# Optimization experiments

Hardware: AMD Instinct MI355X
Metric: run time of the kernel (lower is better)

The kernel has to match this reference:

```python
import jax, jax.numpy as jnp
from jax import lax
import numpy as np

B, T, F = 64, 512, 128
H, L = 256, 128  # hidden_nodes, latent_dim
KEEP = 0.4       # 1 - dropout (dropout = 0.6)


def _lstm_layer(x, W, U, b, mask, return_sequences):
    """Keras-style LSTM (gate order i,f,g,o) with input dropout mask shared over time."""
    xd = x * mask[:, None, :]                       # [B,T,in] * [B,1,in]
    xz = jnp.einsum('bti,ig->btg', xd, W) + b        # [B,T,4H] precomputed input projections
    Hn = U.shape[0]

    def step(carry, xz_t):
        h, c = carry
        z = xz_t + h @ U                             # [B,4H]
        i, f, g, o = jnp.split(z, 4, axis=-1)
        i = jax.nn.sigmoid(i)
        f = jax.nn.sigmoid(f)
        g = jnp.tanh(g)
        o = jax.nn.sigmoid(o)
        c = f * c + i * g
        h = o * jnp.tanh(c)
        return (h, c), h

    init = (jnp.zeros((x.shape[0], Hn), x.dtype), jnp.zeros((x.shape[0], Hn), x.dtype))
    (h_last, _), hs = lax.scan(step, init, jnp.swapaxes(xz, 0, 1))
    return jnp.swapaxes(hs, 0, 1) if return_sequences else h_last


def setup_inputs() -> dict:
    key = jax.random.key(0)
    ks = jax.random.split(key, 16)

    def w(k, shape):
        fan_in = shape[0]
        return (jax.random.normal(k, shape, jnp.float32) / np.sqrt(fan_in)).astype(jnp.float32)

    def dmask(k, shape):
        return (jax.random.bernoulli(k, KEEP, shape).astype(jnp.float32) / KEEP)

    return {
        'x':  jax.random.normal(ks[0], (B, T, F), jnp.float32),
        'W0': w(ks[1], (F, 4 * H)), 'U0': w(ks[2], (H, 4 * H)), 'b0': jnp.zeros((4 * H,), jnp.float32),
        'W1': w(ks[3], (H, 4 * H)), 'U1': w(ks[4], (H, 4 * H)), 'b1': jnp.zeros((4 * H,), jnp.float32),
        'W2': w(ks[5], (H, 4 * L)), 'U2': w(ks[6], (L, 4 * L)), 'b2': jnp.zeros((4 * L,), jnp.float32),
        'm0': dmask(ks[7], (B, F)),
        'm1': dmask(ks[8], (B, H)),
        'm2': dmask(ks[9], (B, H)),
    }


def reference(x, W0, U0, b0, W1, U1, b1, W2, U2, b2, m0, m1, m2):
    h = _lstm_layer(x, W0, U0, b0, m0, return_sequences=True)   # input_layer
    h = _lstm_layer(h, W1, U1, b1, m1, return_sequences=True)   # hidden layer 0
    out = _lstm_layer(h, W2, U2, b2, m2, return_sequences=False)  # output_layer -> [B, latent_dim]
    return out
```

## Files before the change

### kernel.cpp

```cpp
#include <hip/hip_runtime.h>
#include <hip/hip_fp16.h>
#include <math.h>

#define B_ 64
#define T_ 512

typedef _Float16 h2_t __attribute__((ext_vector_type(2)));

__device__ __forceinline__ float fdot2u(unsigned int a, unsigned int b, float c) {
#if __has_builtin(__builtin_amdgcn_fdot2)
    return __builtin_amdgcn_fdot2(__builtin_bit_cast(h2_t, a),
                                  __builtin_bit_cast(h2_t, b), c, false);
#else
    const __half2 ah = __builtin_bit_cast(__half2, a);
    const __half2 bh = __builtin_bit_cast(__half2, b);
    const float2 af = __half22float2(ah), bf = __half22float2(bh);
    return c + af.x * bf.x + af.y * bf.y;
#endif
}
__device__ __forceinline__ unsigned int pack_h2(float x, float y) {
    const __half2 h = __float22half2_rn(make_float2(x, y));
    return __builtin_bit_cast(unsigned int, h);
}
__device__ __forceinline__ float ubits(unsigned int a) { return __builtin_bit_cast(float, a); }
__device__ __forceinline__ unsigned short f2h_bits(float x) {
    return __builtin_bit_cast(unsigned short, (_Float16)x);
}
__device__ __forceinline__ float h2f_bits(unsigned int bits) {
    return (float)__builtin_bit_cast(_Float16, (unsigned short)(bits & 0xffffu));
}

__device__ __forceinline__ float fsig(float z) { return 1.f / (1.f + __expf(-z)); }
__device__ __forceinline__ float ftanh(float z) {
    const float e = __expf(2.f * z);
    return 1.f - 2.f / (e + 1.f);
}

__device__ __forceinline__ void bar_lds() {
    asm volatile("s_waitcnt lgkmcnt(0)" ::: "memory");
    __builtin_amdgcn_s_barrier();
    asm volatile("" ::: "memory");
}

__global__ __launch_bounds__(256) void gemm_mask_f16(
    const float* __restrict__ A, const float* __restrict__ W,
    const float* __restrict__ bias, const float* __restrict__ mask,
    float* __restrict__ C, int M, int N, int K)
{
    const int TM = 64, TN = 64, TK = 32, KP = 16;
    __shared__ __align__(16) unsigned int As2[KP][68];
    __shared__ __align__(16) unsigned int Bs2[KP][68];

    const int tid = threadIdx.x;
    const int bn = blockIdx.x;
    const int bm = blockIdx.y;
    const int row0 = bm * TM;
    const int b = row0 / T_;

    const int ty = tid >> 4;
    const int tx = tid & 15;
    const int m0 = ty * 4;
    const int n0 = tx * 4;

    float acc[4][4];
#pragma unroll
    for (int i = 0; i < 4; i++)
#pragma unroll
        for (int j = 0; j < 4; j++) acc[i][j] = 0.f;

    for (int kk = 0; kk < K; kk += TK) {
        {
            const int m = tid >> 2;
            const int kq = (tid & 3) * 8;
            const float4 mv0 = *(const float4*)(mask + (size_t)b * K + kk + kq);
            const float4 mv1 = *(const float4*)(mask + (size_t)b * K + kk + kq + 4);
            const float4 a0 = *(const float4*)(A + (size_t)(row0 + m) * K + kk + kq);
            const float4 a1 = *(const float4*)(A + (size_t)(row0 + m) * K + kk + kq + 4);
            As2[kq / 2 + 0][m] = pack_h2(a0.x * mv0.x, a0.y * mv0.y);
            As2[kq / 2 + 1][m] = pack_h2(a0.z * mv0.z, a0.w * mv0.w);
            As2[kq / 2 + 2][m] = pack_h2(a1.x * mv1.x, a1.y * mv1.y);
            As2[kq / 2 + 3][m] = pack_h2(a1.z * mv1.z, a1.w * mv1.w);
        }
        {
            const int kp = tid >> 4;
            const int nq = (tid & 15) * 4;
            const float4 w0 = *(const float4*)(W + (size_t)(kk + 2 * kp) * N + bn * TN + nq);
            const float4 w1 = *(const float4*)(W + (size_t)(kk + 2 * kp + 1) * N + bn * TN + nq);
            uint4 pv;
            pv.x = pack_h2(w0.x, w1.x);
            pv.y = pack_h2(w0.y, w1.y);
            pv.z = pack_h2(w0.z, w1.z);
            pv.w = pack_h2(w0.w, w1.w);
            *(uint4*)&Bs2[kp][nq] = pv;
        }
        __syncthreads();

#pragma unroll
        for (int kp = 0; kp < KP; kp++) {
            const uint4 a4 = *(const uint4*)&As2[kp][m0];
            const uint4 b4 = *(const uint4*)&Bs2[kp][n0];
            acc[0][0] = fdot2u(a4.x, b4.x, acc[0][0]); acc[0][1] = fdot2u(a4.x, b4.y, acc[0][1]);
            acc[0][2] = fdot2u(a4.x, b4.z, acc[0][2]); acc[0][3] = fdot2u(a4.x, b4.w, acc[0][3]);
            acc[1][0] = fdot2u(a4.y, b4.x, acc[1][0]); acc[1][1] = fdot2u(a4.y, b4.y, acc[1][1]);
            acc[1][2] = fdot2u(a4.y, b4.z, acc[1][2]); acc[1][3] = fdot2u(a4.y, b4.w, acc[1][3]);
            acc[2][0] = fdot2u(a4.z, b4.x, acc[2][0]); acc[2][1] = fdot2u(a4.z, b4.y, acc[2][1]);
            acc[2][2] = fdot2u(a4.z, b4.z, acc[2][2]); acc[2][3] = fdot2u(a4.z, b4.w, acc[2][3]);
            acc[3][0] = fdot2u(a4.w, b4.x, acc[3][0]); acc[3][1] = fdot2u(a4.w, b4.y, acc[3][1]);
            acc[3][2] = fdot2u(a4.w, b4.z, acc[3][2]); acc[3][3] = fdot2u(a4.w, b4.w, acc[3][3]);
        }
        __syncthreads();
    }

    const float4 bv = *(const float4*)(bias + bn * TN + n0);
#pragma unroll
    for (int i = 0; i < 4; i++) {
        float4 v;
        v.x = acc[i][0] + bv.x;
        v.y = acc[i][1] + bv.y;
        v.z = acc[i][2] + bv.z;
        v.w = acc[i][3] + bv.w;
        *(float4*)&C[(size_t)(row0 + m0 + i) * N + bn * TN + n0] = v;
    }
}

template <int HN, bool F16>
__global__ __launch_bounds__(1024, 4) void lstm_rec_v16(
    const float* __restrict__ xz,
    const float* __restrict__ U,
    float* __restrict__ hout,
    float* __restrict__ out_last,
    unsigned int* __restrict__ hbuf)
{
    constexpr int GATES = 4 * HN;
    constexpr int COLS = HN;
    constexpr int CP = COLS / 2;
    constexpr int NKG = 1024 / CP;
    constexpr int KH = HN / NKG;
    constexpr int HB = HN / 4;
    constexpr int KWORDS = F16 ? HN / 2 : HN;
    constexpr int WPT = F16 ? KH / 2 : KH;
    constexpr int COLSP = COLS + 2;
    constexpr int NR = 3 * HB / 2;

    __shared__ __align__(16) unsigned int hW[KWORDS];
    __shared__ __align__(16) float zpS[NKG * COLSP];

    const int tid = threadIdx.x;
    const int q = blockIdx.x >> 6;
    const int b = blockIdx.x & 63;

    const int cp = tid % CP;
    const int kq = tid / CP;
    const int c0 = 2 * cp;
    const int group = c0 / HB;
    const int gcol = group * HN + q * HB + (c0 % HB);
    const int wbase = kq * WPT;

    uint2 ur[WPT];
#pragma unroll
    for (int j = 0; j < WPT; ++j) {
        const int w = wbase + j;
        if constexpr (F16) {
            const float2 r0 = *(const float2*)(U + (size_t)(2 * w) * GATES + gcol);
            const float2 r1 = *(const float2*)(U + (size_t)(2 * w + 1) * GATES + gcol);
            ur[j].x = pack_h2(r0.x, r1.x);
            ur[j].y = pack_h2(r0.y, r1.y);
        } else {
            const float2 r0 = *(const float2*)(U + (size_t)w * GATES + gcol);
            ur[j].x = __builtin_bit_cast(unsigned int, r0.x);
            ur[j].y = __builtin_bit_cast(unsigned int, r0.y);
        }
    }
#pragma unroll
    for (int j = 0; j < WPT; ++j)
        asm volatile("" : "+v"(ur[j].x), "+v"(ur[j].y));

    if (tid < KWORDS) hW[tid] = 0u;
    float cst = 0.f;

    const float* xzcell = xz + (size_t)b * T_ * GATES + q * HB + tid;
    float z4[4] = {0.f, 0.f, 0.f, 0.f};
    if (tid < HB) {
#pragma unroll
        for (int g = 0; g < 4; ++g) z4[g] = xzcell[(size_t)g * HN];
    }
    __syncthreads();

#pragma unroll 1
    for (int t = 0; t < T_; ++t) {
        float acc0 = 0.f, acc1 = 0.f;
#pragma unroll
        for (int j = 0; j < WPT; j += 4) {
            const int w = wbase + j;
            const uint4 hw4 = *(const uint4*)&hW[w];
            if constexpr (F16) {
                acc0 = fdot2u(ur[j + 0].x, hw4.x, acc0); acc1 = fdot2u(ur[j + 0].y, hw4.x, acc1);
                acc0 = fdot2u(ur[j + 1].x, hw4.y, acc0); acc1 = fdot2u(ur[j + 1].y, hw4.y, acc1);
                acc0 = fdot2u(ur[j + 2].x, hw4.z, acc0); acc1 = fdot2u(ur[j + 2].y, hw4.z, acc1);
                acc0 = fdot2u(ur[j + 3].x, hw4.w, acc0); acc1 = fdot2u(ur[j + 3].y, hw4.w, acc1);
            } else {
                acc0 += ubits(ur[j + 0].x) * ubits(hw4.x); acc1 += ubits(ur[j + 0].y) * ubits(hw4.x);
                acc0 += ubits(ur[j + 1].x) * ubits(hw4.y); acc1 += ubits(ur[j + 1].y) * ubits(hw4.y);
                acc0 += ubits(ur[j + 2].x) * ubits(hw4.z); acc1 += ubits(ur[j + 2].y) * ubits(hw4.z);
                acc0 += ubits(ur[j + 3].x) * ubits(hw4.w); acc1 += ubits(ur[j + 3].y) * ubits(hw4.w);
            }
        }
        *(float2*)&zpS[kq * COLSP + c0] = make_float2(acc0, acc1);
        bar_lds();

        const unsigned int tag = (unsigned int)(t + 1);
        unsigned int* hslot = hbuf + (size_t)(t & 1) * B_ * HN + b * HN;

        if (tid < HB) {
            float zg[4];
#pragma unroll
            for (int g = 0; g < 4; ++g) {
                float zs = z4[g];
#pragma unroll
                for (int r = 0; r < NKG; ++r) zs += zpS[r * COLSP + g * HB + tid];
                zg[g] = zs;
            }
            if (t + 1 < T_) {
#pragma unroll
                for (int g = 0; g < 4; ++g)
                    z4[g] = xzcell[(size_t)(t + 1) * GATES + (size_t)g * HN];
            }
            const float ig = fsig(zg[0]);
            const float fg = fsig(zg[1]);
            const float gg = ftanh(zg[2]);
            const float og = fsig(zg[3]);
            cst = fg * cst + ig * gg;
            const float hnew = og * ftanh(cst);

            if (hout) hout[((size_t)b * T_ + t) * HN + q * HB + tid] = hnew;
            if (t == T_ - 1) {
                if (out_last) out_last[(size_t)b * HN + q * HB + tid] = hnew;
            } else {
                const unsigned short h16 = f2h_bits(hnew);
                __hip_atomic_store(&hslot[q * HB + tid],
                                   ((unsigned int)tag << 16) | (unsigned int)h16,
                                   __ATOMIC_RELAXED, __HIP_MEMORY_SCOPE_AGENT);
                if constexpr (F16) {
                    reinterpret_cast<unsigned short*>(hW)[q * HB + tid] = h16;
                } else {
                    hW[q * HB + tid] = __builtin_bit_cast(unsigned int, hnew);
                }
            }
        } else if (tid >= 64 && tid < 64 + NR && t < T_ - 1) {
            const int idx = tid - 64;
            const int qp0 = q * (HB / 2);
            const int p = idx + (idx >= qp0 ? (HB / 2) : 0);
            const unsigned long long* hq = (const unsigned long long*)hslot;
            unsigned long long v = __hip_atomic_load(&hq[p],
                __ATOMIC_RELAXED, __HIP_MEMORY_SCOPE_AGENT);
            while (((v >> 16) & 0xffffu) != tag || (v >> 48) != tag)
                v = __hip_atomic_load(&hq[p],
                    __ATOMIC_RELAXED, __HIP_MEMORY_SCOPE_AGENT);
            if constexpr (F16) {
                hW[p] = (unsigned int)(v & 0xffffu) |
                        ((unsigned int)((v >> 32) & 0xffffu) << 16);
            } else {
                hW[2 * p + 0] = __builtin_bit_cast(unsigned int, h2f_bits((unsigned int)v));
                hW[2 * p + 1] = __builtin_bit_cast(unsigned int, h2f_bits((unsigned int)(v >> 32)));
            }
        }
        bar_lds();
    }
}

__global__ __launch_bounds__(1024, 4) void lstm_full_v18(
    const float* __restrict__ xz,
    const float* __restrict__ U,
    float* __restrict__ out_last)
{
    constexpr int HN = 128;
    constexpr int GATES = 512;
    constexpr int COLS = 512;
    constexpr int CP = COLS / 2;
    constexpr int NKG = 1024 / CP;
    constexpr int KH = HN / NKG;
    constexpr int WPT = KH;
    constexpr int KWORDS = HN;
    constexpr int COLSP = COLS + 2;

    __shared__ __align__(16) unsigned int hW[KWORDS];
    __shared__ __align__(16) float zpS[NKG * COLSP];

    const int tid = threadIdx.x;
    const int b = blockIdx.x;

    const int cp = tid % CP;
    const int kq = tid / CP;
    const int c0 = 2 * cp;
    const int wbase = kq * WPT;

    uint2 ur[WPT];
#pragma unroll
    for (int j = 0; j < WPT; ++j) {
        const int w = wbase + j;
        const float2 r0 = *(const float2*)(U + (size_t)w * GATES + c0);
        ur[j].x = __builtin_bit_cast(unsigned int, r0.x);
        ur[j].y = __builtin_bit_cast(unsigned int, r0.y);
    }
#pragma unroll
    for (int j = 0; j < WPT; ++j)
        asm volatile("" : "+v"(ur[j].x), "+v"(ur[j].y));

    if (tid < KWORDS) hW[tid] = 0u;
    float cst = 0.f;

    const float* xzcell = xz + (size_t)b * T_ * GATES + tid;
    float z4[4] = {0.f, 0.f, 0.f, 0.f};
    if (tid < HN) {
#pragma unroll
        for (int g = 0; g < 4; ++g) z4[g] = xzcell[g * HN];
    }
    __syncthreads();

#pragma unroll 1
    for (int t = 0; t < T_; ++t) {
        float acc0 = 0.f, acc1 = 0.f;
#pragma unroll
        for (int j = 0; j < WPT; j += 4) {
            const int w = wbase + j;
            const uint4 hw4 = *(const uint4*)&hW[w];
            acc0 += ubits(ur[j + 0].x) * ubits(hw4.x); acc1 += ubits(ur[j + 0].y) * ubits(hw4.x);
            acc0 += ubits(ur[j + 1].x) * ubits(hw4.y); acc1 += ubits(ur[j + 1].y) * ubits(hw4.y);
            acc0 += ubits(ur[j + 2].x) * ubits(hw4.z); acc1 += ubits(ur[j + 2].y) * ubits(hw4.z);
            acc0 += ubits(ur[j + 3].x) * ubits(hw4.w); acc1 += ubits(ur[j + 3].y) * ubits(hw4.w);
        }
        *(float2*)&zpS[kq * COLSP + c0] = make_float2(acc0, acc1);
        bar_lds();

        if (tid < HN) {
            float zg[4];
#pragma unroll
            for (int g = 0; g < 4; ++g) {
                float zs = z4[g];
#pragma unroll
                for (int r = 0; r < NKG; ++r) zs += zpS[r * COLSP + g * HN + tid];
                zg[g] = zs;
            }
            if (t + 1 < T_) {
#pragma unroll
                for (int g = 0; g < 4; ++g)
                    z4[g] = xzcell[(size_t)(t + 1) * GATES + g * HN];
            }
            const float ig = fsig(zg[0]);
            const float fg = fsig(zg[1]);
            const float gg = ftanh(zg[2]);
            const float og = fsig(zg[3]);
            cst = fg * cst + ig * gg;
            const float hnew = og * ftanh(cst);

            if (t == T_ - 1) {
                out_last[(size_t)b * HN + tid] = hnew;
            } else {
                hW[tid] = __builtin_bit_cast(unsigned int, hnew);
            }
        }
        bar_lds();
    }
}

extern "C" void kernel_launch(void* const* d_in, const int* in_sizes, int n_in,
                              void* d_out, int out_size, void* d_ws, size_t ws_size,
                              hipStream_t stream)
{
    const float* x  = (const float*)d_in[0];
    const float* W0 = (const float*)d_in[1];
    const float* U0 = (const float*)d_in[2];
    const float* b0 = (const float*)d_in[3];
    const float* W1 = (const float*)d_in[4];
    const float* U1 = (const float*)d_in[5];
    const float* b1 = (const float*)d_in[6];
    const float* W2 = (const float*)d_in[7];
    const float* U2 = (const float*)d_in[8];
    const float* b2 = (const float*)d_in[9];
    const float* m0 = (const float*)d_in[10];
    const float* m1 = (const float*)d_in[11];
    const float* m2 = (const float*)d_in[12];
    float* out = (float*)d_out;

    char* ws = (char*)d_ws;
    float* xz = (float*)ws;
    float* h0 = (float*)(ws + 134217728);
    float* h1 = (float*)(ws + 134217728 + 33554432);
    unsigned int* hb0 = (unsigned int*)(ws + 134217728 + 2 * 33554432);
    unsigned int* hb1 = hb0 + 2 * B_ * 256;

    const int M = B_ * T_;

    gemm_mask_f16<<<dim3(1024 / 64, M / 64), 256, 0, stream>>>(x, W0, b0, m0, xz, M, 1024, 128);
    lstm_rec_v16<256, true><<<256, 1024, 0, stream>>>(xz, U0, h0, nullptr, hb0);

    gemm_mask_f16<<<dim3(1024 / 64, M / 64), 256, 0, stream>>>(h0, W1, b1, m1, xz, M, 1024, 256);
    lstm_rec_v16<256, true><<<256, 1024, 0, stream>>>(xz, U1, h1, nullptr, hb1);

    gemm_mask_f16<<<dim3(512 / 64, M / 64), 256, 0, stream>>>(h1, W2, b2, m2, xz, M, 512, 256);
    lstm_full_v18<<<64, 1024, 0, stream>>>(xz, U2, out);
}
```

Before: 2.114 ms.

## Replace fdot2 input-projection GEMM with MFMA f16 matrix-core GEMM

Rewrites the masked input-projection GEMM to use MFMA 16x16x32 f16 instructions, with 128x128 block tiles split into four 64x64 wave tiles and a K-major LDS layout for both operands. The goal is to move the three large projection GEMMs off scalar packed-dot arithmetic and onto the matrix cores. The trade-offs are scattered 4-byte output stores in place of float4 stores, strided scalar loads of W, and fewer blocks per GEMM. The sequential recurrent kernels, which likely dominate total time, are unchanged.

```diff
diff --git a/kernel.cpp b/kernel.cpp
--- a/kernel.cpp
+++ b/kernel.cpp
@@ -6,6 +6,8 @@
 #define T_ 512
 
 typedef _Float16 h2_t __attribute__((ext_vector_type(2)));
+typedef _Float16 f16x8 __attribute__((ext_vector_type(8)));
+typedef float f32x4 __attribute__((ext_vector_type(4)));
 
 __device__ __forceinline__ float fdot2u(unsigned int a, unsigned int b, float c) {
 #if __has_builtin(__builtin_amdgcn_fdot2)
@@ -42,84 +44,100 @@
     asm volatile("" ::: "memory");
 }
 
-__global__ __launch_bounds__(256) void gemm_mask_f16(
+__global__ __launch_bounds__(256) void gemm_mask_mfma(
     const float* __restrict__ A, const float* __restrict__ W,
     const float* __restrict__ bias, const float* __restrict__ mask,
     float* __restrict__ C, int M, int N, int K)
 {
-    const int TM = 64, TN = 64, TK = 32, KP = 16;
-    __shared__ __align__(16) unsigned int As2[KP][68];
-    __shared__ __align__(16) unsigned int Bs2[KP][68];
+    __shared__ __align__(16) unsigned int AsT[128][20];
+    __shared__ __align__(16) unsigned int BsT[128][20];
 
     const int tid = threadIdx.x;
     const int bn = blockIdx.x;
     const int bm = blockIdx.y;
-    const int row0 = bm * TM;
+    const int row0 = bm * 128;
+    const int col0 = bn * 128;
     const int b = row0 / T_;
 
-    const int ty = tid >> 4;
-    const int tx = tid & 15;
-    const int m0 = ty * 4;
-    const int n0 = tx * 4;
-
-    float acc[4][4];
-#pragma unroll
-    for (int i = 0; i < 4; i++)
-#pragma unroll
-        for (int j = 0; j < 4; j++) acc[i][j] = 0.f;
-
-    for (int kk = 0; kk < K; kk += TK) {
+    const int wave = tid >> 6;
+    const int lane = tid & 63;
+    const int wm = (wave >> 1) * 64;
+    const int wn = (wave & 1) * 64;
+    const int lr = lane & 15;
+    const int g  = lane >> 4;
+
+    f32x4 acc[4][4];
+#pragma unroll
+    for (int i = 0; i < 4; ++i)
+#pragma unroll
+        for (int j = 0; j < 4; ++j) acc[i][j] = (f32x4){0.f, 0.f, 0.f, 0.f};
+
+    for (int kk = 0; kk < K; kk += 32) {
         {
-            const int m = tid >> 2;
-            const int kq = (tid & 3) * 8;
-            const float4 mv0 = *(const float4*)(mask + (size_t)b * K + kk + kq);
-            const float4 mv1 = *(const float4*)(mask + (size_t)b * K + kk + kq + 4);
-            const float4 a0 = *(const float4*)(A + (size_t)(row0 + m) * K + kk + kq);
-            const float4 a1 = *(const float4*)(A + (size_t)(row0 + m) * K + kk + kq + 4);
-            As2[kq / 2 + 0][m] = pack_h2(a0.x * mv0.x, a0.y * mv0.y);
-            As2[kq / 2 + 1][m] = pack_h2(a0.z * mv0.z, a0.w * mv0.w);
-            As2[kq / 2 + 2][m] = pack_h2(a1.x * mv1.x, a1.y * mv1.y);
-            As2[kq / 2 + 3][m] = pack_h2(a1.z * mv1.z, a1.w * mv1.w);
+            const int m = tid >> 1;
+            const int half = tid & 1;
+            const float* ap = A + (size_t)(row0 + m) * K + kk + half * 16;
+            const float* mp = mask + (size_t)b * K + kk + half * 16;
+            const float4 a0 = *(const float4*)(ap);
+            const float4 a1 = *(const float4*)(ap + 4);
+            const float4 a2 = *(const float4*)(ap + 8);
+            const float4 a3 = *(const float4*)(ap + 12);
+            const float4 m0 = *(const float4*)(mp);
+            const float4 m1 = *(const float4*)(mp + 4);
+            const float4 m2 = *(const float4*)(mp + 8);
+            const float4 m3 = *(const float4*)(mp + 12);
+            uint4 lo, hi;
+            lo.x = pack_h2(a0.x * m0.x, a0.y * m0.y);
+            lo.y = pack_h2(a0.z * m0.z, a0.w * m0.w);
+            lo.z = pack_h2(a1.x * m1.x, a1.y * m1.y);
+            lo.w = pack_h2(a1.z * m1.z, a1.w * m1.w);
+            hi.x = pack_h2(a2.x * m2.x, a2.y * m2.y);
+            hi.y = pack_h2(a2.z * m2.z, a2.w * m2.w);
+            hi.z = pack_h2(a3.x * m3.x, a3.y * m3.y);
+            hi.w = pack_h2(a3.z * m3.z, a3.w * m3.w);
+            *(uint4*)&AsT[m][half * 8 + 0] = lo;
+            *(uint4*)&AsT[m][half * 8 + 4] = hi;
         }
         {
             const int kp = tid >> 4;
-            const int nq = (tid & 15) * 4;
-            const float4 w0 = *(const float4*)(W + (size_t)(kk + 2 * kp) * N + bn * TN + nq);
-            const float4 w1 = *(const float4*)(W + (size_t)(kk + 2 * kp + 1) * N + bn * TN + nq);
-            uint4 pv;
-            pv.x = pack_h2(w0.x, w1.x);
-            pv.y = pack_h2(w0.y, w1.y);
-            pv.z = pack_h2(w0.z, w1.z);
-            pv.w = pack_h2(w0.w, w1.w);
-            *(uint4*)&Bs2[kp][nq] = pv;
+            const int t15 = tid & 15;
+            const float* w0p = W + (size_t)(kk + 2 * kp) * N + col0 + t15;
+            const float* w1p = W + (size_t)(kk + 2 * kp + 1) * N + col0 + t15;
+#pragma unroll
+            for (int i = 0; i < 8; ++i) {
+                const int n = t15 + 16 * i;
+                BsT[n][kp] = pack_h2(w0p[16 * i], w1p[16 * i]);
+            }
         }
         __syncthreads();
 
-#pragma unroll
-        for (int kp = 0; kp < KP; kp++) {
-            const uint4 a4 = *(const uint4*)&As2[kp][m0];
-            const uint4 b4 = *(const uint4*)&Bs2[kp][n0];
-            acc[0][0] = fdot2u(a4.x, b4.x, acc[0][0]); acc[0][1] = fdot2u(a4.x, b4.y, acc[0][1]);
-            acc[0][2] = fdot2u(a4.x, b4.z, acc[0][2]); acc[0][3] = fdot2u(a4.x, b4.w, acc[0][3]);
-            acc[1][0] = fdot2u(a4.y, b4.x, acc[1][0]); acc[1][1] = fdot2u(a4.y, b4.y, acc[1][1]);
-            acc[1][2] = fdot2u(a4.y, b4.z, acc[1][2]); acc[1][3] = fdot2u(a4.y, b4.w, acc[1][3]);
-            acc[2][0] = fdot2u(a4.z, b4.x, acc[2][0]); acc[2][1] = fdot2u(a4.z, b4.y, acc[2][1]);
-            acc[2][2] = fdot2u(a4.z, b4.z, acc[2][2]); acc[2][3] = fdot2u(a4.z, b4.w, acc[2][3]);
-            acc[3][0] = fdot2u(a4.w, b4.x, acc[3][0]); acc[3][1] = fdot2u(a4.w, b4.y, acc[3][1]);
-            acc[3][2] = fdot2u(a4.w, b4.z, acc[3][2]); acc[3][3] = fdot2u(a4.w, b4.w, acc[3][3]);
-        }
+        f16x8 af[4], bf[4];
+#pragma unroll
+        for (int i = 0; i < 4; ++i)
+            af[i] = __builtin_bit_cast(f16x8, *(const uint4*)&AsT[wm + 16 * i + lr][g * 4]);
+#pragma unroll
+        for (int j = 0; j < 4; ++j)
+            bf[j] = __builtin_bit_cast(f16x8, *(const uint4*)&BsT[wn + 16 * j + lr][g * 4]);
+#pragma unroll
+        for (int i = 0; i < 4; ++i)
+#pragma unroll
+            for (int j = 0; j < 4; ++j)
+                acc[i][j] = __builtin_amdgcn_mfma_f32_16x16x32_f16(af[i], bf[j], acc[i][j], 0, 0, 0);
         __syncthreads();
     }
 
-    const float4 bv = *(const float4*)(bias + bn * TN + n0);
-#pragma unroll
-    for (int i = 0; i < 4; i++) {
-        float4 v;
-        v.x = acc[i][0] + bv.x;
-        v.y = acc[i][1] + bv.y;
-        v.z = acc[i][2] + bv.z;
-        v.w = acc[i][3] + bv.w;
-        *(float4*)&C[(size_t)(row0 + m0 + i) * N + bn * TN + n0] = v;
+#pragma unroll
+    for (int j = 0; j < 4; ++j) {
+        const int c = col0 + wn + 16 * j + lr;
+        const float bv = bias[c];
+#pragma unroll
+        for (int i = 0; i < 4; ++i) {
+            const int r0 = row0 + wm + 16 * i + g * 4;
+            C[(size_t)(r0 + 0) * N + c] = acc[i][j][0] + bv;
+            C[(size_t)(r0 + 1) * N + c] = acc[i][j][1] + bv;
+            C[(size_t)(r0 + 2) * N + c] = acc[i][j][2] + bv;
+            C[(size_t)(r0 + 3) * N + c] = acc[i][j][3] + bv;
+        }
     }
 }
 
@@ -391,12 +409,12 @@
 
     const int M = B_ * T_;
 
-    gemm_mask_f16<<<dim3(1024 / 64, M / 64), 256, 0, stream>>>(x, W0, b0, m0, xz, M, 1024, 128);
+    gemm_mask_mfma<<<dim3(1024 / 128, M / 128), 256, 0, stream>>>(x, W0, b0, m0, xz, M, 1024, 128);
     lstm_rec_v16<256, true><<<256, 1024, 0, stream>>>(xz, U0, h0, nullptr, hb0);
 
-    gemm_mask_f16<<<dim3(1024 / 64, M / 64), 256, 0, stream>>>(h0, W1, b1, m1, xz, M, 1024, 256);
+    gemm_mask_mfma<<<dim3(1024 / 128, M / 128), 256, 0, stream>>>(h0, W1, b1, m1, xz, M, 1024, 256);
     lstm_rec_v16<256, true><<<256, 1024, 0, stream>>>(xz, U1, h1, nullptr, hb1);
 
-    gemm_mask_f16<<<dim3(512 / 64, M / 64), 256, 0, stream>>>(h1, W2, b2, m2, xz, M, 512, 256);
+    gemm_mask_mfma<<<dim3(512 / 128, M / 128), 256, 0, stream>>>(h1, W2, b2, m2, xz, M, 512, 256);
     lstm_full_v18<<<64, 1024, 0, stream>>>(xz, U2, out);
 }
```

After: 1.971 ms (median of 2 runs). 6.8% less time.
